# Optimization experiments

Measured on AMD Instinct MI355X. Metric: run time of the kernel, lower is better.

Reference implementation:

```python
import jax, jax.numpy as jnp
import numpy as np

B, S, D = 4, 2048, 1024
H = 16
HD = D // H

def setup_inputs() -> dict:
    key = jax.random.key(0)
    ks = jax.random.split(key, 6)
    std = 1.0 / np.sqrt(D)
    x = jax.random.normal(ks[0], (B, S, D), dtype=jnp.float32)
    Wq = jax.random.uniform(ks[1], (D, D), jnp.float32, -std, std)
    Wk = jax.random.uniform(ks[2], (D, D), jnp.float32, -std, std)
    Wv = jax.random.uniform(ks[3], (D, D), jnp.float32, -std, std)
    Wo = jax.random.uniform(ks[4], (D, D), jnp.float32, -std, std)
    bo = jax.random.uniform(ks[5], (D,), jnp.float32, -std, std)
    return {"x": x, "Wq": Wq, "Wk": Wk, "Wv": Wv, "Wo": Wo, "bo": bo}

def reference(x, Wq, Wk, Wv, Wo, bo):
    b, s, _ = x.shape
    # projections; torch Linear computes x @ W^T, here W stored as (d_in, d_out)... we use (D, D) applied as x @ W
    q = (x @ Wq).reshape(b, s, H, HD).transpose(0, 2, 1, 3)  # b h s hd
    k = (x @ Wk).reshape(b, s, H, HD).transpose(0, 2, 1, 3)
    v = (x @ Wv).reshape(b, s, H, HD).transpose(0, 2, 1, 3)
    scores = jnp.einsum('bhqd,bhkd->bhqk', q, k)
    causal = jnp.triu(jnp.ones((s, s), dtype=bool), k=1)
    scores = jnp.where(causal[None, None], -jnp.inf, scores)
    attn = jax.nn.softmax(scores / np.sqrt(HD), axis=-1)  # dropout=0.0 -> identity
    ctx = jnp.einsum('bhqk,bhkd->bhqd', attn, v)
    ctx = ctx.transpose(0, 2, 1, 3).reshape(b, s, D)
    return ctx @ Wo + bo
```

## Files before the change

kernel.cpp:

```cpp
#include <hip/hip_runtime.h>

typedef unsigned short u16;
typedef __bf16 bf16x8 __attribute__((ext_vector_type(8)));
typedef float f32x4 __attribute__((ext_vector_type(4)));

#define Bn 4
#define Sn 2048
#define Dn 1024
#define Hn 16
#define HDn 64

__device__ inline u16 f2bf(float f) {
  unsigned u = __builtin_bit_cast(unsigned, f);
  u += 0x7fffu + ((u >> 16) & 1u);
  return (u16)(u >> 16);
}

__device__ __forceinline__ void gl2lds16(const u16* g, u16* l) {
  __builtin_amdgcn_global_load_lds(
      (const __attribute__((address_space(1))) unsigned int*)g,
      (__attribute__((address_space(3))) unsigned int*)l, 16, 0, 0);
}

__device__ __forceinline__ float fexp2(float x) {
  return __builtin_amdgcn_exp2f(x);
}

__device__ __forceinline__ unsigned pk_bf_trunc(float lo, float hi) {
  return __builtin_amdgcn_perm(__builtin_bit_cast(unsigned, hi),
                               __builtin_bit_cast(unsigned, lo), 0x07060302u);
}

__global__ __launch_bounds__(256) void cvt4(const float* __restrict__ in,
                                            u16* __restrict__ out, int n4) {
  int i = blockIdx.x * 256 + threadIdx.x;
  if (i < n4) {
    float4 v = ((const float4*)in)[i];
    ushort4 o;
    o.x = f2bf(v.x); o.y = f2bf(v.y); o.z = f2bf(v.z); o.w = f2bf(v.w);
    ((ushort4*)out)[i] = o;
  }
}

__global__ __launch_bounds__(256) void tcvt4(const float* __restrict__ w0,
                                             const float* __restrict__ w1,
                                             const float* __restrict__ w2,
                                             const float* __restrict__ w3,
                                             u16* __restrict__ out) {
  __shared__ u16 tile[32][33];
  const float* in = (blockIdx.z == 0) ? w0 : (blockIdx.z == 1) ? w1
                   : (blockIdx.z == 2) ? w2 : w3;
  u16* dst = out + (size_t)blockIdx.z * Dn * Dn;
  int bx = blockIdx.x * 32;
  int by = blockIdx.y * 32;
  int tx = threadIdx.x & 31;
  int ty = threadIdx.x >> 5;
#pragma unroll
  for (int r = 0; r < 32; r += 8)
    tile[ty + r][tx] = f2bf(in[(size_t)(by + ty + r) * Dn + bx + tx]);
  __syncthreads();
#pragma unroll
  for (int r = 0; r < 32; r += 8)
    dst[(size_t)(bx + ty + r) * Dn + by + tx] = tile[tx][ty + r];
}

__global__ __launch_bounds__(256) void gemm_qkv(const u16* __restrict__ A,
                                                const u16* __restrict__ Bt,
                                                u16* __restrict__ qb,
                                                u16* __restrict__ kb,
                                                u16* __restrict__ vt,
                                                float qscale) {
  __shared__ __attribute__((aligned(16))) u16 As[2][2][128][32];
  __shared__ __attribute__((aligned(16))) u16 Bs[2][2][128][32];
  const int K = Dn;
  const int t = threadIdx.x;
  const int wave = t >> 6;
  const int lane = t & 63;
  const int lcol = lane & 15;
  const int quad = lane >> 4;
  const int wm = (wave >> 1) * 64;
  const int wn = (wave & 1) * 64;
  const int bm = blockIdx.y * 128;
  const int bn = blockIdx.x * 128;

  const int srow = lane >> 2;
  const int sseg = (lane & 3) * 8;
  const u16* a0p = A + (size_t)(bm + wave * 16 + srow) * K + sseg;
  const u16* a1p = a0p + (size_t)64 * K;
  const u16* b0p = Bt + (size_t)(bn + wave * 16 + srow) * K + sseg;
  const u16* b1p = b0p + (size_t)64 * K;
  u16* asl = &As[0][0][0][0] + wave * 512 + lane * 8;
  u16* bsl = &Bs[0][0][0][0] + wave * 512 + lane * 8;

  auto stage = [&](int k0, int d) {
    u16* as = asl + d * 8192;
    u16* bs = bsl + d * 8192;
    gl2lds16(a0p + k0, as);
    gl2lds16(a1p + k0, as + 2048);
    gl2lds16(a0p + k0 + 32, as + 4096);
    gl2lds16(a1p + k0 + 32, as + 6144);
    gl2lds16(b0p + k0, bs);
    gl2lds16(b1p + k0, bs + 2048);
    gl2lds16(b0p + k0 + 32, bs + 4096);
    gl2lds16(b1p + k0 + 32, bs + 6144);
  };

  f32x4 acc[4][4];
#pragma unroll
  for (int i = 0; i < 4; i++)
#pragma unroll
    for (int j = 0; j < 4; j++) acc[i][j] = (f32x4){0.f, 0.f, 0.f, 0.f};

  stage(0, 0);
  int d = 0;
  for (int k0 = 0; k0 < K; k0 += 64, d ^= 1) {
    __syncthreads();
    if (k0 + 64 < K) stage(k0 + 64, d ^ 1);
#pragma unroll
    for (int ks = 0; ks < 2; ks++) {
      bf16x8 af[4], bf[4];
#pragma unroll
      for (int mi = 0; mi < 4; mi++)
        af[mi] = *(const bf16x8*)(&As[d][ks][wm + mi * 16 + lcol][quad * 8]);
#pragma unroll
      for (int ni = 0; ni < 4; ni++)
        bf[ni] = *(const bf16x8*)(&Bs[d][ks][wn + ni * 16 + lcol][quad * 8]);
#pragma unroll
      for (int mi = 0; mi < 4; mi++)
#pragma unroll
        for (int ni = 0; ni < 4; ni++)
          acc[mi][ni] = __builtin_amdgcn_mfma_f32_16x16x32_bf16(af[mi], bf[ni], acc[mi][ni], 0, 0, 0);
    }
  }

  if (bn >= 2048) {
    const int b = bm >> 11;
#pragma unroll
    for (int mi = 0; mi < 4; mi++) {
#pragma unroll
      for (int ni = 0; ni < 4; ni++) {
        int row0 = bm + wm + mi * 16 + quad * 4;
        int s = row0 & (Sn - 1);
        int vcol = bn + wn + ni * 16 + lcol - 2048;
        int bh = (b << 4) + (vcol >> 6);
        int hd = vcol & 63;
        unsigned d0 = (unsigned)f2bf(acc[mi][ni][0]) |
                      ((unsigned)f2bf(acc[mi][ni][1]) << 16);
        unsigned d1 = (unsigned)f2bf(acc[mi][ni][2]) |
                      ((unsigned)f2bf(acc[mi][ni][3]) << 16);
        *(uint2*)(vt + ((size_t)bh * HDn + hd) * Sn + s) = (uint2){d0, d1};
      }
    }
  } else {
    const bool isq = (bn < 1024);
    u16* dst = isq ? qb : kb;
    const int coff = isq ? bn : bn - 1024;
    const float scale = isq ? qscale : 1.0f;
#pragma unroll
    for (int mi = 0; mi < 4; mi++) {
#pragma unroll
      for (int ni = 0; ni < 4; ni++) {
#pragma unroll
        for (int r = 0; r < 4; r++) {
          int row = bm + wm + mi * 16 + quad * 4 + r;
          int col = coff + wn + ni * 16 + lcol;
          dst[(size_t)row * Dn + col] = f2bf(acc[mi][ni][r] * scale);
        }
      }
    }
  }
}

__global__ __launch_bounds__(256) void gemm_out(const u16* __restrict__ A,
                                                const u16* __restrict__ Bt,
                                                float* __restrict__ Cout,
                                                const float* __restrict__ bias) {
  __shared__ __attribute__((aligned(16))) u16 As[2][2][128][32];
  __shared__ __attribute__((aligned(16))) u16 Bs[2][2][128][32];
  const int K = Dn;
  const int t = threadIdx.x;
  const int wave = t >> 6;
  const int lane = t & 63;
  const int lcol = lane & 15;
  const int quad = lane >> 4;
  const int wm = (wave >> 1) * 64;
  const int wn = (wave & 1) * 64;
  const int bm = blockIdx.y * 128;
  const int bn = blockIdx.x * 128;

  const int srow = lane >> 2;
  const int sseg = (lane & 3) * 8;
  const u16* a0p = A + (size_t)(bm + wave * 16 + srow) * K + sseg;
  const u16* a1p = a0p + (size_t)64 * K;
  const u16* b0p = Bt + (size_t)(bn + wave * 16 + srow) * K + sseg;
  const u16* b1p = b0p + (size_t)64 * K;
  u16* asl = &As[0][0][0][0] + wave * 512 + lane * 8;
  u16* bsl = &Bs[0][0][0][0] + wave * 512 + lane * 8;

  auto stage = [&](int k0, int d) {
    u16* as = asl + d * 8192;
    u16* bs = bsl + d * 8192;
    gl2lds16(a0p + k0, as);
    gl2lds16(a1p + k0, as + 2048);
    gl2lds16(a0p + k0 + 32, as + 4096);
    gl2lds16(a1p + k0 + 32, as + 6144);
    gl2lds16(b0p + k0, bs);
    gl2lds16(b1p + k0, bs + 2048);
    gl2lds16(b0p + k0 + 32, bs + 4096);
    gl2lds16(b1p + k0 + 32, bs + 6144);
  };

  f32x4 acc[4][4];
#pragma unroll
  for (int i = 0; i < 4; i++)
#pragma unroll
    for (int j = 0; j < 4; j++) acc[i][j] = (f32x4){0.f, 0.f, 0.f, 0.f};

  stage(0, 0);
  int d = 0;
  for (int k0 = 0; k0 < K; k0 += 64, d ^= 1) {
    __syncthreads();
    if (k0 + 64 < K) stage(k0 + 64, d ^ 1);
#pragma unroll
    for (int ks = 0; ks < 2; ks++) {
      bf16x8 af[4], bf[4];
#pragma unroll
      for (int mi = 0; mi < 4; mi++)
        af[mi] = *(const bf16x8*)(&As[d][ks][wm + mi * 16 + lcol][quad * 8]);
#pragma unroll
      for (int ni = 0; ni < 4; ni++)
        bf[ni] = *(const bf16x8*)(&Bs[d][ks][wn + ni * 16 + lcol][quad * 8]);
#pragma unroll
      for (int mi = 0; mi < 4; mi++)
#pragma unroll
        for (int ni = 0; ni < 4; ni++)
          acc[mi][ni] = __builtin_amdgcn_mfma_f32_16x16x32_bf16(af[mi], bf[ni], acc[mi][ni], 0, 0, 0);
    }
  }

#pragma unroll
  for (int mi = 0; mi < 4; mi++) {
#pragma unroll
    for (int ni = 0; ni < 4; ni++) {
#pragma unroll
      for (int r = 0; r < 4; r++) {
        int row = bm + wm + mi * 16 + quad * 4 + r;
        int col = bn + wn + ni * 16 + lcol;
        Cout[(size_t)row * Dn + col] = acc[mi][ni][r] + bias[col];
      }
    }
  }
}

__global__ __launch_bounds__(256, 2) void attn6(const u16* __restrict__ Qb,
                                                const u16* __restrict__ Kb,
                                                const u16* __restrict__ Vt,
                                                u16* __restrict__ ctx) {
  __shared__ __attribute__((aligned(16))) u16 Ks2[2][2][64][32];
  __shared__ __attribute__((aligned(16))) u16 Vts2[2][2][64][32];
  __shared__ __attribute__((aligned(16))) u16 Pt[4][32][72];

  const int bh = blockIdx.x;
  const int b = bh >> 4, h = bh & 15;
  const int pair = blockIdx.y;
  const int t = threadIdx.x;
  const int w = t >> 6;
  const int lane = t & 63;
  const int lcol = lane & 15;
  const int quad = lane >> 4;
  const int qw0 = pair * 128 + w * 32;
  const int qw1 = (15 - pair) * 128 + w * 32;

  const size_t base = ((size_t)b * Sn) * Dn + h * HDn;
  const size_t vbase = ((size_t)bh * HDn) * Sn;

  bf16x8 qf[2][2][2];
#pragma unroll
  for (int si = 0; si < 2; si++) {
    const int qws = si ? qw1 : qw0;
#pragma unroll
    for (int qb = 0; qb < 2; qb++) {
      const u16* qp = Qb + base + (size_t)(qws + qb * 16 + lcol) * Dn + quad * 8;
      qf[si][qb][0] = *(const bf16x8*)qp;
      qf[si][qb][1] = *(const bf16x8*)(qp + 32);
    }
  }

  f32x4 o[2][2][4];
#pragma unroll
  for (int si = 0; si < 2; si++)
#pragma unroll
    for (int qb = 0; qb < 2; qb++)
#pragma unroll
      for (int nb = 0; nb < 4; nb++) o[si][qb][nb] = (f32x4){0.f, 0.f, 0.f, 0.f};
  float lsum[2][2] = {{0.f, 0.f}, {0.f, 0.f}};

  const int srow = lane >> 2;
  const int sseg = (lane & 3) * 8;
  const u16* kp0 = Kb + base + (size_t)(w * 16 + srow) * Dn + sseg;
  const u16* vp0 = Vt + vbase + (size_t)(w * 16 + srow) * Sn + sseg;
  u16* ksl = &Ks2[0][0][0][0] + w * 512 + lane * 8;
  u16* vsl = &Vts2[0][0][0][0] + w * 512 + lane * 8;

  auto stage = [&](int j0, int dd) {
    const u16* kp = kp0 + (size_t)j0 * Dn;
    gl2lds16(kp, ksl + dd * 4096);
    gl2lds16(kp + 32, ksl + dd * 4096 + 2048);
    const u16* vp = vp0 + j0;
    gl2lds16(vp, vsl + dd * 4096);
    gl2lds16(vp + 32, vsl + dd * 4096 + 2048);
  };

  auto do_strip = [&](int si, int qw, int j0, int dd) {
    f32x4 s[4][2];
#pragma unroll
    for (int mb = 0; mb < 4; mb++) {
      bf16x8 kf0 = *(const bf16x8*)(&Ks2[dd][0][mb * 16 + lcol][quad * 8]);
      bf16x8 kf1 = *(const bf16x8*)(&Ks2[dd][1][mb * 16 + lcol][quad * 8]);
#pragma unroll
      for (int qb = 0; qb < 2; qb++) {
        f32x4 a = (f32x4){0.f, 0.f, 0.f, 0.f};
        a = __builtin_amdgcn_mfma_f32_16x16x32_bf16(kf0, qf[si][qb][0], a, 0, 0, 0);
        a = __builtin_amdgcn_mfma_f32_16x16x32_bf16(kf1, qf[si][qb][1], a, 0, 0, 0);
        s[mb][qb] = a;
      }
    }

    const bool needmask = (j0 + 63 > qw);
#pragma unroll
    for (int qb = 0; qb < 2; qb++) {
      const int qrow = qw + qb * 16 + lcol;
#pragma unroll
      for (int mb = 0; mb < 4; mb++) {
        float p[4];
#pragma unroll
        for (int r = 0; r < 4; r++) p[r] = fexp2(s[mb][qb][r]);
        if (needmask) {
          const int kvb = j0 + mb * 16 + quad * 4;
#pragma unroll
          for (int r = 0; r < 4; r++)
            if (kvb + r > qrow) p[r] = 0.f;
        }
        lsum[si][qb] += (p[0] + p[1]) + (p[2] + p[3]);
        unsigned d0 = pk_bf_trunc(p[0], p[1]);
        unsigned d1 = pk_bf_trunc(p[2], p[3]);
        *(uint2*)(&Pt[w][qb * 16 + lcol][mb * 16 + quad * 4]) = (uint2){d0, d1};
      }
    }

#pragma unroll
    for (int c = 0; c < 2; c++) {
      bf16x8 pf0 = *(const bf16x8*)(&Pt[w][lcol][c * 32 + quad * 8]);
      bf16x8 pf1 = *(const bf16x8*)(&Pt[w][16 + lcol][c * 32 + quad * 8]);
#pragma unroll
      for (int nb = 0; nb < 4; nb++) {
        bf16x8 vf = *(const bf16x8*)(&Vts2[dd][c][nb * 16 + lcol][quad * 8]);
        o[si][0][nb] = __builtin_amdgcn_mfma_f32_16x16x32_bf16(vf, pf0, o[si][0][nb], 0, 0, 0);
        o[si][1][nb] = __builtin_amdgcn_mfma_f32_16x16x32_bf16(vf, pf1, o[si][1][nb], 0, 0, 0);
      }
    }
  };

  const int n_kv = (15 - pair) * 128 + 128;

  stage(0, 0);
  int d = 0;
  for (int j0 = 0; j0 < n_kv; j0 += 64, d ^= 1) {
    __syncthreads();
    if (j0 + 64 < n_kv) stage(j0 + 64, d ^ 1);
    if (j0 <= qw1 + 31) do_strip(1, qw1, j0, d);
    if (j0 <= qw0 + 31) do_strip(0, qw0, j0, d);
  }

#pragma unroll
  for (int si = 0; si < 2; si++) {
    const int qws = si ? qw1 : qw0;
#pragma unroll
    for (int qb = 0; qb < 2; qb++) {
      float l = lsum[si][qb];
      l += __shfl_xor(l, 16);
      l += __shfl_xor(l, 32);
      float inv = 1.0f / l;
#pragma unroll
      for (int nb = 0; nb < 4; nb++) {
        unsigned d0 = (unsigned)f2bf(o[si][qb][nb][0] * inv) |
                      ((unsigned)f2bf(o[si][qb][nb][1] * inv) << 16);
        unsigned d1 = (unsigned)f2bf(o[si][qb][nb][2] * inv) |
                      ((unsigned)f2bf(o[si][qb][nb][3] * inv) << 16);
        u16* p = ctx + base + (size_t)(qws + qb * 16 + lcol) * Dn + nb * 16 + quad * 4;
        *(uint2*)p = (uint2){d0, d1};
      }
    }
  }
}

extern "C" void kernel_launch(void* const* d_in, const int* in_sizes, int n_in,
                              void* d_out, int out_size, void* d_ws, size_t ws_size,
                              hipStream_t stream) {
  const float* x  = (const float*)d_in[0];
  const float* Wq = (const float*)d_in[1];
  const float* Wk = (const float*)d_in[2];
  const float* Wv = (const float*)d_in[3];
  const float* Wo = (const float*)d_in[4];
  const float* bo = (const float*)d_in[5];
  float* out = (float*)d_out;

  const size_t BSD = (size_t)Bn * Sn * Dn;
  const size_t DD = (size_t)Dn * Dn;

  u16* xb   = (u16*)d_ws;
  u16* wall = xb + BSD;
  u16* qb   = wall + 4 * DD;
  u16* kb   = qb + BSD;
  u16* vt   = kb + BSD;
  u16* cb   = vt + BSD;

  cvt4<<<(int)(BSD / 4 / 256), 256, 0, stream>>>(x, xb, (int)(BSD / 4));
  tcvt4<<<dim3(Dn / 32, Dn / 32, 4), 256, 0, stream>>>(Wq, Wk, Wv, Wo, wall);

  gemm_qkv<<<dim3(3072 / 128, (Bn * Sn) / 128), 256, 0, stream>>>(
      xb, wall, qb, kb, vt, 0.125f * 1.44269504f);

  attn6<<<dim3(Bn * Hn, 8), 256, 0, stream>>>(qb, kb, vt, cb);

  gemm_out<<<dim3(Dn / 128, (Bn * Sn) / 128), 256, 0, stream>>>(cb, wall + 3 * DD, out, bo);
}
```

Measured before the change: 241.4 us.

## Split attention into one query block per workgroup with higher occupancy

The attention kernel no longer pairs query blocks i and 15-i in one workgroup. It now handles a single 128-row query block per workgroup and launches twice as many workgroups, largest first, with launch bounds raised to 4 blocks per CU. The K/V double buffering is replaced by a single shared-memory buffer that is loaded and then synchronized each iteration, so the kernel relies on extra resident waves to hide load latency. In exchange, each K/V tile is no longer reused across two strips, which raises total K/V traffic, and every iteration now pays two barriers.

```diff
diff --git a/kernel.cpp b/kernel.cpp
--- a/kernel.cpp
+++ b/kernel.cpp
@@ -252,144 +252,130 @@
   }
 }
 
-__global__ __launch_bounds__(256, 2) void attn6(const u16* __restrict__ Qb,
+__global__ __launch_bounds__(256, 4) void attn7(const u16* __restrict__ Qb,
                                                 const u16* __restrict__ Kb,
                                                 const u16* __restrict__ Vt,
                                                 u16* __restrict__ ctx) {
-  __shared__ __attribute__((aligned(16))) u16 Ks2[2][2][64][32];
-  __shared__ __attribute__((aligned(16))) u16 Vts2[2][2][64][32];
+  __shared__ __attribute__((aligned(16))) u16 Ks2[2][64][32];
+  __shared__ __attribute__((aligned(16))) u16 Vts2[2][64][32];
   __shared__ __attribute__((aligned(16))) u16 Pt[4][32][72];
 
   const int bh = blockIdx.x;
   const int b = bh >> 4, h = bh & 15;
-  const int pair = blockIdx.y;
+  const int q0 = (15 - blockIdx.y) * 128;
   const int t = threadIdx.x;
   const int w = t >> 6;
   const int lane = t & 63;
   const int lcol = lane & 15;
   const int quad = lane >> 4;
-  const int qw0 = pair * 128 + w * 32;
-  const int qw1 = (15 - pair) * 128 + w * 32;
+  const int qw = q0 + w * 32;
 
   const size_t base = ((size_t)b * Sn) * Dn + h * HDn;
   const size_t vbase = ((size_t)bh * HDn) * Sn;
 
-  bf16x8 qf[2][2][2];
-#pragma unroll
-  for (int si = 0; si < 2; si++) {
-    const int qws = si ? qw1 : qw0;
-#pragma unroll
-    for (int qb = 0; qb < 2; qb++) {
-      const u16* qp = Qb + base + (size_t)(qws + qb * 16 + lcol) * Dn + quad * 8;
-      qf[si][qb][0] = *(const bf16x8*)qp;
-      qf[si][qb][1] = *(const bf16x8*)(qp + 32);
-    }
-  }
-
-  f32x4 o[2][2][4];
-#pragma unroll
-  for (int si = 0; si < 2; si++)
-#pragma unroll
-    for (int qb = 0; qb < 2; qb++)
-#pragma unroll
-      for (int nb = 0; nb < 4; nb++) o[si][qb][nb] = (f32x4){0.f, 0.f, 0.f, 0.f};
-  float lsum[2][2] = {{0.f, 0.f}, {0.f, 0.f}};
+  bf16x8 qf[2][2];
+#pragma unroll
+  for (int qb_ = 0; qb_ < 2; qb_++) {
+    const u16* qp = Qb + base + (size_t)(qw + qb_ * 16 + lcol) * Dn + quad * 8;
+    qf[qb_][0] = *(const bf16x8*)qp;
+    qf[qb_][1] = *(const bf16x8*)(qp + 32);
+  }
+
+  f32x4 o[2][4];
+#pragma unroll
+  for (int qb_ = 0; qb_ < 2; qb_++)
+#pragma unroll
+    for (int nb = 0; nb < 4; nb++) o[qb_][nb] = (f32x4){0.f, 0.f, 0.f, 0.f};
+  float lsum[2] = {0.f, 0.f};
 
   const int srow = lane >> 2;
   const int sseg = (lane & 3) * 8;
   const u16* kp0 = Kb + base + (size_t)(w * 16 + srow) * Dn + sseg;
   const u16* vp0 = Vt + vbase + (size_t)(w * 16 + srow) * Sn + sseg;
-  u16* ksl = &Ks2[0][0][0][0] + w * 512 + lane * 8;
-  u16* vsl = &Vts2[0][0][0][0] + w * 512 + lane * 8;
-
-  auto stage = [&](int j0, int dd) {
-    const u16* kp = kp0 + (size_t)j0 * Dn;
-    gl2lds16(kp, ksl + dd * 4096);
-    gl2lds16(kp + 32, ksl + dd * 4096 + 2048);
-    const u16* vp = vp0 + j0;
-    gl2lds16(vp, vsl + dd * 4096);
-    gl2lds16(vp + 32, vsl + dd * 4096 + 2048);
-  };
-
-  auto do_strip = [&](int si, int qw, int j0, int dd) {
-    f32x4 s[4][2];
-#pragma unroll
-    for (int mb = 0; mb < 4; mb++) {
-      bf16x8 kf0 = *(const bf16x8*)(&Ks2[dd][0][mb * 16 + lcol][quad * 8]);
-      bf16x8 kf1 = *(const bf16x8*)(&Ks2[dd][1][mb * 16 + lcol][quad * 8]);
-#pragma unroll
-      for (int qb = 0; qb < 2; qb++) {
-        f32x4 a = (f32x4){0.f, 0.f, 0.f, 0.f};
-        a = __builtin_amdgcn_mfma_f32_16x16x32_bf16(kf0, qf[si][qb][0], a, 0, 0, 0);
-        a = __builtin_amdgcn_mfma_f32_16x16x32_bf16(kf1, qf[si][qb][1], a, 0, 0, 0);
-        s[mb][qb] = a;
-      }
-    }
-
-    const bool needmask = (j0 + 63 > qw);
-#pragma unroll
-    for (int qb = 0; qb < 2; qb++) {
-      const int qrow = qw + qb * 16 + lcol;
+  u16* ksl0 = &Ks2[0][0][0] + w * 512 + lane * 8;
+  u16* ksl1 = ksl0 + 2048;
+  u16* vsl0 = &Vts2[0][0][0] + w * 512 + lane * 8;
+  u16* vsl1 = vsl0 + 2048;
+
+  const int n_kv = q0 + 128;
+
+  for (int j0 = 0; j0 < n_kv; j0 += 64) {
+    {
+      const u16* kp = kp0 + (size_t)j0 * Dn;
+      gl2lds16(kp, ksl0);
+      gl2lds16(kp + 32, ksl1);
+      const u16* vp = vp0 + j0;
+      gl2lds16(vp, vsl0);
+      gl2lds16(vp + 32, vsl1);
+    }
+    __syncthreads();
+
+    if (j0 <= qw + 31) {
+      f32x4 s[4][2];
 #pragma unroll
       for (int mb = 0; mb < 4; mb++) {
-        float p[4];
-#pragma unroll
-        for (int r = 0; r < 4; r++) p[r] = fexp2(s[mb][qb][r]);
-        if (needmask) {
-          const int kvb = j0 + mb * 16 + quad * 4;
-#pragma unroll
-          for (int r = 0; r < 4; r++)
-            if (kvb + r > qrow) p[r] = 0.f;
+        bf16x8 kf0 = *(const bf16x8*)(&Ks2[0][mb * 16 + lcol][quad * 8]);
+        bf16x8 kf1 = *(const bf16x8*)(&Ks2[1][mb * 16 + lcol][quad * 8]);
+#pragma unroll
+        for (int qb_ = 0; qb_ < 2; qb_++) {
+          f32x4 a = (f32x4){0.f, 0.f, 0.f, 0.f};
+          a = __builtin_amdgcn_mfma_f32_16x16x32_bf16(kf0, qf[qb_][0], a, 0, 0, 0);
+          a = __builtin_amdgcn_mfma_f32_16x16x32_bf16(kf1, qf[qb_][1], a, 0, 0, 0);
+          s[mb][qb_] = a;
         }
-        lsum[si][qb] += (p[0] + p[1]) + (p[2] + p[3]);
-        unsigned d0 = pk_bf_trunc(p[0], p[1]);
-        unsigned d1 = pk_bf_trunc(p[2], p[3]);
-        *(uint2*)(&Pt[w][qb * 16 + lcol][mb * 16 + quad * 4]) = (uint2){d0, d1};
-      }
-    }
-
-#pragma unroll
-    for (int c = 0; c < 2; c++) {
-      bf16x8 pf0 = *(const bf16x8*)(&Pt[w][lcol][c * 32 + quad * 8]);
-      bf16x8 pf1 = *(const bf16x8*)(&Pt[w][16 + lcol][c * 32 + quad * 8]);
-#pragma unroll
-      for (int nb = 0; nb < 4; nb++) {
-        bf16x8 vf = *(const bf16x8*)(&Vts2[dd][c][nb * 16 + lcol][quad * 8]);
-        o[si][0][nb] = __builtin_amdgcn_mfma_f32_16x16x32_bf16(vf, pf0, o[si][0][nb], 0, 0, 0);
-        o[si][1][nb] = __builtin_amdgcn_mfma_f32_16x16x32_bf16(vf, pf1, o[si][1][nb], 0, 0, 0);
-      }
-    }
-  };
-
-  const int n_kv = (15 - pair) * 128 + 128;
-
-  stage(0, 0);
-  int d = 0;
-  for (int j0 = 0; j0 < n_kv; j0 += 64, d ^= 1) {
+      }
+
+      const bool needmask = (j0 + 63 > qw);
+#pragma unroll
+      for (int qb_ = 0; qb_ < 2; qb_++) {
+        const int qrow = qw + qb_ * 16 + lcol;
+#pragma unroll
+        for (int mb = 0; mb < 4; mb++) {
+          float p[4];
+#pragma unroll
+          for (int r = 0; r < 4; r++) p[r] = fexp2(s[mb][qb_][r]);
+          if (needmask) {
+            const int kvb = j0 + mb * 16 + quad * 4;
+#pragma unroll
+            for (int r = 0; r < 4; r++)
+              if (kvb + r > qrow) p[r] = 0.f;
+          }
+          lsum[qb_] += (p[0] + p[1]) + (p[2] + p[3]);
+          unsigned d0 = pk_bf_trunc(p[0], p[1]);
+          unsigned d1 = pk_bf_trunc(p[2], p[3]);
+          *(uint2*)(&Pt[w][qb_ * 16 + lcol][mb * 16 + quad * 4]) = (uint2){d0, d1};
+        }
+      }
+
+#pragma unroll
+      for (int c = 0; c < 2; c++) {
+        bf16x8 pf0 = *(const bf16x8*)(&Pt[w][lcol][c * 32 + quad * 8]);
+        bf16x8 pf1 = *(const bf16x8*)(&Pt[w][16 + lcol][c * 32 + quad * 8]);
+#pragma unroll
+        for (int nb = 0; nb < 4; nb++) {
+          bf16x8 vf = *(const bf16x8*)(&Vts2[c][nb * 16 + lcol][quad * 8]);
+          o[0][nb] = __builtin_amdgcn_mfma_f32_16x16x32_bf16(vf, pf0, o[0][nb], 0, 0, 0);
+          o[1][nb] = __builtin_amdgcn_mfma_f32_16x16x32_bf16(vf, pf1, o[1][nb], 0, 0, 0);
+        }
+      }
+    }
     __syncthreads();
-    if (j0 + 64 < n_kv) stage(j0 + 64, d ^ 1);
-    if (j0 <= qw1 + 31) do_strip(1, qw1, j0, d);
-    if (j0 <= qw0 + 31) do_strip(0, qw0, j0, d);
-  }
-
-#pragma unroll
-  for (int si = 0; si < 2; si++) {
-    const int qws = si ? qw1 : qw0;
-#pragma unroll
-    for (int qb = 0; qb < 2; qb++) {
-      float l = lsum[si][qb];
-      l += __shfl_xor(l, 16);
-      l += __shfl_xor(l, 32);
-      float inv = 1.0f / l;
-#pragma unroll
-      for (int nb = 0; nb < 4; nb++) {
-        unsigned d0 = (unsigned)f2bf(o[si][qb][nb][0] * inv) |
-                      ((unsigned)f2bf(o[si][qb][nb][1] * inv) << 16);
-        unsigned d1 = (unsigned)f2bf(o[si][qb][nb][2] * inv) |
-                      ((unsigned)f2bf(o[si][qb][nb][3] * inv) << 16);
-        u16* p = ctx + base + (size_t)(qws + qb * 16 + lcol) * Dn + nb * 16 + quad * 4;
-        *(uint2*)p = (uint2){d0, d1};
-      }
+  }
+
+#pragma unroll
+  for (int qb_ = 0; qb_ < 2; qb_++) {
+    float l = lsum[qb_];
+    l += __shfl_xor(l, 16);
+    l += __shfl_xor(l, 32);
+    float inv = 1.0f / l;
+#pragma unroll
+    for (int nb = 0; nb < 4; nb++) {
+      unsigned d0 = (unsigned)f2bf(o[qb_][nb][0] * inv) |
+                    ((unsigned)f2bf(o[qb_][nb][1] * inv) << 16);
+      unsigned d1 = (unsigned)f2bf(o[qb_][nb][2] * inv) |
+                    ((unsigned)f2bf(o[qb_][nb][3] * inv) << 16);
+      u16* p = ctx + base + (size_t)(qw + qb_ * 16 + lcol) * Dn + nb * 16 + quad * 4;
+      *(uint2*)p = (uint2){d0, d1};
     }
   }
 }
@@ -421,7 +407,7 @@
   gemm_qkv<<<dim3(3072 / 128, (Bn * Sn) / 128), 256, 0, stream>>>(
       xb, wall, qb, kb, vt, 0.125f * 1.44269504f);
 
-  attn6<<<dim3(Bn * Hn, 8), 256, 0, stream>>>(qb, kb, vt, cb);
+  attn7<<<dim3(Bn * Hn, 16), 256, 0, stream>>>(qb, kb, vt, cb);
 
   gemm_out<<<dim3(Dn / 128, (Bn * Sn) / 128), 256, 0, stream>>>(cb, wall + 3 * DD, out, bo);
 }
```

Result: no change. 242.6 us (+0.5%).
